# Optimization experiments

Measured on AMD Instinct MI355X. Metric: run time of the kernel, lower is better.

## Reference

```python
import jax, jax.numpy as jnp
import numpy as np

STEP = 16      # step_size
WIN = 8        # causal window width from attn_mask
NUM_HEADS = 4
LN_EPS = 1e-5


def conv1d(x, w, b, pad, dil):
    # x: [B, Cin, T], w: [Cout, Cin, K] (torch layout)
    y = jax.lax.conv_general_dilated(
        x, w, window_strides=(1,), padding=[(pad, pad)],
        rhs_dilation=(dil,), dimension_numbers=('NCH', 'OIH', 'NCH'))
    return y + b[None, :, None]


def temporal_block(x, w1, b1, w2, b2, wd, bd, dil, pad):
    # Canonical TCN block: conv->chomp->relu (dropout=eval noop) x2 + residual
    T = x.shape[-1]
    out = jax.nn.relu(conv1d(x, w1, b1, pad, dil)[..., :T])
    out = jax.nn.relu(conv1d(out, w2, b2, pad, dil)[..., :T])
    res = x if wd is None else conv1d(x, wd, bd, 0, 1)
    return jax.nn.relu(out + res)


def layer_norm(x, g, b):
    m = x.mean(-1, keepdims=True)
    v = x.var(-1, keepdims=True)
    return (x - m) / jnp.sqrt(v + LN_EPS) * g + b


def setup_inputs() -> dict:
    key = jax.random.key(0)
    NOISE, HID, B, T = 128, 256, 32, 4096
    ks = iter(jax.random.split(key, 48))
    rn = lambda shape, s=0.05: jax.random.normal(next(ks), shape, jnp.float32) * s
    inp = {'z': jax.random.normal(next(ks), (B, NOISE, T), jnp.float32)}
    # TCN block 0: kernel 1, noise_dim -> hidden_dim, with 1x1 downsample
    inp['tb0_w1'] = rn((HID, NOISE, 1)); inp['tb0_b1'] = jnp.zeros(HID)
    inp['tb0_w2'] = rn((HID, HID, 1));   inp['tb0_b2'] = jnp.zeros(HID)
    inp['tb0_wd'] = rn((HID, NOISE, 1)); inp['tb0_bd'] = jnp.zeros(HID)
    # TCN blocks 1..3: kernel 2, dilations 1,2,4, same channels (identity residual)
    for i in (1, 2, 3):
        inp[f'tb{i}_w1'] = rn((HID, HID, 2)); inp[f'tb{i}_b1'] = jnp.zeros(HID)
        inp[f'tb{i}_w2'] = rn((HID, HID, 2)); inp[f'tb{i}_b2'] = jnp.zeros(HID)
    # MultiheadAttention params (torch layout)
    inp['attn_in_w'] = rn((3 * HID, HID)); inp['attn_in_b'] = jnp.zeros(3 * HID)
    inp['attn_out_w'] = rn((HID, HID));    inp['attn_out_b'] = jnp.zeros(HID)
    inp['ln1_g'] = jnp.ones(HID); inp['ln1_b'] = jnp.zeros(HID)
    inp['ln2_g'] = jnp.ones(HID); inp['ln2_b'] = jnp.zeros(HID)
    inp['ffn_w1'] = rn((2 * HID, HID)); inp['ffn_b1'] = jnp.zeros(2 * HID)
    inp['ffn_w2'] = rn((HID, 2 * HID)); inp['ffn_b2'] = jnp.zeros(HID)
    inp['last_w'] = rn((1, HID)); inp['last_b'] = jnp.zeros(1)
    return inp


def reference(z, tb0_w1, tb0_b1, tb0_w2, tb0_b2, tb0_wd, tb0_bd,
              tb1_w1, tb1_b1, tb1_w2, tb1_b2,
              tb2_w1, tb2_b1, tb2_w2, tb2_b2,
              tb3_w1, tb3_b1, tb3_w2, tb3_b2,
              attn_in_w, attn_in_b, attn_out_w, attn_out_b,
              ln1_g, ln1_b, ln2_g, ln2_b,
              ffn_w1, ffn_b1, ffn_w2, ffn_b2,
              last_w, last_b):
    # --- TCN stack ---
    z = temporal_block(z, tb0_w1, tb0_b1, tb0_w2, tb0_b2, tb0_wd, tb0_bd, 1, 0)
    z = temporal_block(z, tb1_w1, tb1_b1, tb1_w2, tb1_b2, None, None, 1, 1)
    z = temporal_block(z, tb2_w1, tb2_b1, tb2_w2, tb2_b2, None, None, 2, 2)
    z = temporal_block(z, tb3_w1, tb3_b1, tb3_w2, tb3_b2, None, None, 4, 4)
    B, C, T = z.shape
    S = T // STEP
    # [B,C,S,STEP] -> [B,STEP,S,C] -> [B*STEP, S, C]
    x = z.reshape(B, C, S, STEP).transpose(0, 3, 2, 1).reshape(B * STEP, S, C)
    # --- causal sliding-window MHA ---
    qkv = x @ attn_in_w.T + attn_in_b
    q, k, v = jnp.split(qkv, 3, axis=-1)
    H, Dh = NUM_HEADS, C // NUM_HEADS
    heads = lambda t: t.reshape(B * STEP, S, H, Dh).transpose(0, 2, 1, 3)
    q, k, v = heads(q), heads(k), heads(v)
    scale = 1.0 / float(np.sqrt(Dh))
    scores = jnp.einsum('bhqd,bhkd->bhqk', q, k) * scale
    i = jnp.arange(S)[:, None]; j = jnp.arange(S)[None, :]
    allowed = (i - j >= 0) & (i - j < WIN)   # masked where i-j<0 or i-j>=8
    scores = jnp.where(allowed, scores, -jnp.inf)
    attn = jax.nn.softmax(scores, axis=-1)
    o = jnp.einsum('bhqk,bhkd->bhqd', attn, v)
    o = o.transpose(0, 2, 1, 3).reshape(B * STEP, S, C)
    o = o @ attn_out_w.T + attn_out_b
    # --- residual + LN + FFN + LN (dropout = eval noop) ---
    x = layer_norm(x + o, ln1_g, ln1_b)
    f = jax.nn.gelu(x @ ffn_w1.T + ffn_b1, approximate=False) @ ffn_w2.T + ffn_b2
    x = layer_norm(x + f, ln2_g, ln2_b)
    # un-fold back to [B, C, T]
    z = x.reshape(B, STEP, S, C).transpose(0, 3, 2, 1).reshape(B, C, T)
    out = z.transpose(0, 2, 1) @ last_w.T + last_b  # [B, T, 1]
    return out.transpose(0, 2, 1)                    # [B, 1, T]
```

## Files before the change

kernel.cpp:

```cpp
#include <hip/hip_runtime.h>
#include <cmath>

#define BB 32
#define TT 4096

typedef unsigned short u16;
typedef __attribute__((ext_vector_type(8))) __bf16 bf16x8;
typedef __attribute__((ext_vector_type(4))) float f32x4;
typedef __attribute__((ext_vector_type(8))) unsigned short u16x8;
typedef __attribute__((ext_vector_type(4))) unsigned short u16x4;
typedef __attribute__((ext_vector_type(2))) unsigned short u16x2;
typedef __attribute__((ext_vector_type(4))) unsigned int u32x4;

typedef __attribute__((address_space(3))) unsigned int lds_uint;
typedef __attribute__((address_space(1))) unsigned int g_uint;

__device__ __forceinline__ void gl_lds16(const void* g, void* l) {
    __builtin_amdgcn_global_load_lds((const g_uint*)g, (lds_uint*)l, 16, 0, 0);
}

__device__ __forceinline__ u16 f2b(float x) {
    unsigned u = __builtin_bit_cast(unsigned, x);
    return (u16)((u + 0x7fffu + ((u >> 16) & 1u)) >> 16);
}
__device__ __forceinline__ float b2f(u16 h) {
    unsigned u = ((unsigned)h) << 16;
    return __builtin_bit_cast(float, u);
}
__device__ __forceinline__ unsigned pkbf(float a, float b) {
    unsigned ua = __builtin_bit_cast(unsigned, a) + 0x8000u;
    unsigned ub = __builtin_bit_cast(unsigned, b) + 0x8000u;
    return __builtin_amdgcn_perm(ub, ua, 0x07060302);
}

enum : int {
  W_TB0_1 = 0,
  W_TB0_2 = 32768,
  W_TB0_D = 98304,
  W_TB1_1_T0 = 131072, W_TB1_1_T1 = 196608,
  W_TB1_2_T0 = 262144, W_TB1_2_T1 = 327680,
  W_TB2_1_T0 = 393216, W_TB2_1_T1 = 458752,
  W_TB2_2_T0 = 524288, W_TB2_2_T1 = 589824,
  W_TB3_1_T0 = 655360, W_TB3_1_T1 = 720896,
  W_TB3_2_T0 = 786432, W_TB3_2_T1 = 851968,
  W_ATTN_IN  = 917504,
  W_ATTN_OUT = 1114112,
  W_FFN1     = 1179648,
  W_FFN2     = 1310720,
};

__global__ __launch_bounds__(256)
void prep_weights(const float* s0, const float* s1, const float* s2,
                  const float* s3, const float* s4, const float* s5,
                  const float* s6, const float* s7, const float* s8,
                  const float* s9, const float* s10, const float* s11,
                  const float* s12, u16* wb)
{
    int seg = blockIdx.y;
    int i = blockIdx.x * 256 + threadIdx.x;
    switch (seg) {
    case 0:  if (i < 32768)  wb[W_TB0_1 + i] = f2b(s0[i]); break;
    case 1:  if (i < 65536)  wb[W_TB0_2 + i] = f2b(s1[i]); break;
    case 2:  if (i < 32768)  wb[W_TB0_D + i] = f2b(s2[i]); break;
    case 3:  if (i < 65536) { wb[W_TB1_1_T0 + i] = f2b(s3[2*i]); wb[W_TB1_1_T1 + i] = f2b(s3[2*i+1]); } break;
    case 4:  if (i < 65536) { wb[W_TB1_2_T0 + i] = f2b(s4[2*i]); wb[W_TB1_2_T1 + i] = f2b(s4[2*i+1]); } break;
    case 5:  if (i < 65536) { wb[W_TB2_1_T0 + i] = f2b(s5[2*i]); wb[W_TB2_1_T1 + i] = f2b(s5[2*i+1]); } break;
    case 6:  if (i < 65536) { wb[W_TB2_2_T0 + i] = f2b(s6[2*i]); wb[W_TB2_2_T1 + i] = f2b(s6[2*i+1]); } break;
    case 7:  if (i < 65536) { wb[W_TB3_1_T0 + i] = f2b(s7[2*i]); wb[W_TB3_1_T1 + i] = f2b(s7[2*i+1]); } break;
    case 8:  if (i < 65536) { wb[W_TB3_2_T0 + i] = f2b(s8[2*i]); wb[W_TB3_2_T1 + i] = f2b(s8[2*i+1]); } break;
    case 9:  if (i < 196608) wb[W_ATTN_IN + i]  = f2b(s9[i]);  break;
    case 10: if (i < 65536)  wb[W_ATTN_OUT + i] = f2b(s10[i]); break;
    case 11: if (i < 131072) wb[W_FFN1 + i]     = f2b(s11[i]); break;
    case 12: if (i < 131072) wb[W_FFN2 + i]     = f2b(s12[i]); break;
    }
}

__global__ __launch_bounds__(256)
void transpose_z(const float* __restrict__ z, u16* __restrict__ Z)
{
    __shared__ u16 tile[64][33];
    const int t0 = blockIdx.x << 6;
    const int c0 = blockIdx.y << 5;
    const int b  = blockIdx.z;
    const int tid = threadIdx.x;
    #pragma unroll
    for (int r = 0; r < 8; r++) {
        int lin = r * 256 + tid;
        int cc = lin >> 6, tt = lin & 63;
        tile[tt][cc] = f2b(z[((size_t)b * 128 + c0 + cc) * TT + t0 + tt]);
    }
    __syncthreads();
    #pragma unroll
    for (int r = 0; r < 8; r++) {
        int lin = r * 256 + tid;
        int tt = lin >> 5, cc = lin & 31;
        Z[((size_t)b * TT + t0 + tt) * 128 + c0 + cc] = tile[tt][cc];
    }
}

__device__ __forceinline__ const bf16x8* lds_frag(const u16* base, int row, int lc) {
    return (const bf16x8*)((const char*)base + row * 128 + (((lc ^ row) & 7) << 4) + ((lc & ~7) << 4));
}

template<int ACT, bool DUAL, int RMODE>
__global__ __launch_bounds__(256)
void gemm_tok(const u16* __restrict__ X, const u16* __restrict__ W1, int K,
              const u16* __restrict__ W2, int sh,
              const float* __restrict__ bias1,
              const u16* __restrict__ res, u16* __restrict__ Y, int M,
              const u16* __restrict__ zp)
{
    constexpr int XR = DUAL ? 132 : 128;
    constexpr int WR = DUAL ? 256 : 128;
    constexpr int WU = WR / 32;
    constexpr int STB = (XR + WR) * 128;
    constexpr int SMB = STB > 33792 ? STB : 33792;
    __shared__ __align__(16) char smem[SMB];
    u16* Xs = (u16*)smem;
    u16* Ws = (u16*)(smem + XR * 128);
    float (*CT)[132] = (float(*)[132])smem;

    const int tid = threadIdx.x;
    const int b  = blockIdx.z;
    const int t0 = blockIdx.x << 7;
    const int n0 = blockIdx.y << 7;
    const int lane = tid & 63;
    const int wv = tid >> 6;
    const int wt = (wv >> 1) << 6;
    const int wn = (wv & 1) << 6;
    const int l15 = lane & 15;
    const int quad = lane >> 4;
    const int shl = DUAL ? sh : 0;

    const char* xsrc[4]; char* xdst[4];
    #pragma unroll
    for (int u = 0; u < 4; u++) {
        const int c = tid + (u << 8);
        const int r = c >> 3, p = c & 7, q = p ^ (r & 7);
        const int st = t0 + r - shl;
        xdst[u] = (char*)Xs + c * 16;
        xsrc[u] = (const char*)((st >= 0 ? (X + ((size_t)b * TT + st) * K) : zp) + q * 8);
    }
    const char* wsrc[WU]; char* wdst[WU];
    #pragma unroll
    for (int u = 0; u < WU; u++) {
        const int c = tid + (u << 8);
        const int r = c >> 3, p = c & 7, q = p ^ (r & 7);
        wdst[u] = (char*)Ws + c * 16;
        const u16* wb_ = (DUAL && r >= 128) ? (W2 + (size_t)(n0 + r - 128) * K)
                                            : (W1 + (size_t)(n0 + r) * K);
        wsrc[u] = (const char*)(wb_ + q * 8);
    }
    const u16* hsrc = nullptr; u16* hdst = nullptr;
    if (DUAL && tid < 8 * shl) {
        const int hr = 128 + (tid >> 3), hp = tid & 7, hq = hp ^ (hr & 7);
        hsrc = X + ((size_t)b * TT + t0 + hr - shl) * K + hq * 8;
        hdst = (u16*)((char*)Xs + (1024 + tid) * 16);
    }

    f32x4 acc[4][4];
    #pragma unroll
    for (int j = 0; j < 4; j++) {
        const f32x4 bj = *(const f32x4*)&bias1[n0 + wn + j * 16 + quad * 4];
        #pragma unroll
        for (int i = 0; i < 4; i++) acc[i][j] = bj;
    }

    for (int k0 = 0; k0 < K; k0 += 64) {
        #pragma unroll
        for (int u = 0; u < 4; u++) gl_lds16(xsrc[u] + 2 * k0, xdst[u]);
        #pragma unroll
        for (int u = 0; u < WU; u++) gl_lds16(wsrc[u] + 2 * k0, wdst[u]);
        if (DUAL && hdst) *(u16x8*)hdst = *(const u16x8*)(hsrc + k0);
        __syncthreads();
        #pragma unroll
        for (int ks = 0; ks < 2; ks++) {
            bf16x8 af[4], bw[4];
            const int lc = ks * 4 + quad;
            #pragma unroll
            for (int i = 0; i < 4; i++)
                af[i] = *lds_frag(Xs, shl + wt + i * 16 + l15, lc);
            #pragma unroll
            for (int j = 0; j < 4; j++)
                bw[j] = *lds_frag(Ws, wn + j * 16 + l15, lc);
            #pragma unroll
            for (int i = 0; i < 4; i++)
                #pragma unroll
                for (int j = 0; j < 4; j++)
                    acc[i][j] = __builtin_amdgcn_mfma_f32_16x16x32_bf16(bw[j], af[i], acc[i][j], 0, 0, 0);
            if (DUAL) {
                #pragma unroll
                for (int i = 0; i < 4; i++)
                    af[i] = *lds_frag(Xs, wt + i * 16 + l15, lc);
                #pragma unroll
                for (int j = 0; j < 4; j++)
                    bw[j] = *lds_frag(Ws, 128 + wn + j * 16 + l15, lc);
                #pragma unroll
                for (int i = 0; i < 4; i++)
                    #pragma unroll
                    for (int j = 0; j < 4; j++)
                        acc[i][j] = __builtin_amdgcn_mfma_f32_16x16x32_bf16(bw[j], af[i], acc[i][j], 0, 0, 0);
            }
        }
        __syncthreads();
    }

    #pragma unroll
    for (int h = 0; h < 2; h++) {
        if (wt == h * 64) {
            #pragma unroll
            for (int i = 0; i < 4; i++) {
                const int tt = i * 16 + l15;
                #pragma unroll
                for (int j = 0; j < 4; j++)
                    *(f32x4*)&CT[tt][wn + j * 16 + quad * 4] = acc[i][j];
            }
        }
        __syncthreads();
        #pragma unroll
        for (int r4 = 0; r4 < 4; r4++) {
            const int lin = (r4 << 8) + tid;
            const int tt = lin >> 4;
            const int ck = lin & 15;
            const int gr = t0 + h * 64 + tt;
            const int gc = n0 + ck * 8;
            const size_t oidx = ((size_t)b * TT + gr) * M + gc;
            f32x4 v0 = *(const f32x4*)&CT[tt][ck * 8];
            f32x4 v1 = *(const f32x4*)&CT[tt][ck * 8 + 4];
            if (RMODE) {
                const u16x8 rv = *(const u16x8*)&res[oidx];
                if (RMODE == 2) {
                    #pragma unroll
                    for (int e = 0; e < 4; e++) {
                        v0[e] = fmaxf(fmaxf(v0[e], 0.f) + b2f(rv[e]), 0.f);
                        v1[e] = fmaxf(fmaxf(v1[e], 0.f) + b2f(rv[e + 4]), 0.f);
                    }
                } else {
                    #pragma unroll
                    for (int e = 0; e < 4; e++) { v0[e] += b2f(rv[e]); v1[e] += b2f(rv[e + 4]); }
                }
            }
            if (RMODE != 2) {
                if (ACT == 1) {
                    #pragma unroll
                    for (int e = 0; e < 4; e++) { v0[e] = fmaxf(v0[e], 0.f); v1[e] = fmaxf(v1[e], 0.f); }
                }
                if (ACT == 2) {
                    #pragma unroll
                    for (int e = 0; e < 4; e++) {
                        v0[e] = 0.5f * v0[e] * (1.f + erff(v0[e] * 0.70710678118f));
                        v1[e] = 0.5f * v1[e] * (1.f + erff(v1[e] * 0.70710678118f));
                    }
                }
            }
            u32x4 po;
            po[0] = pkbf(v0[0], v0[1]);
            po[1] = pkbf(v0[2], v0[3]);
            po[2] = pkbf(v1[0], v1[1]);
            po[3] = pkbf(v1[2], v1[3]);
            *(u32x4*)&Y[oidx] = po;
        }
        if (h == 0) __syncthreads();
    }
}

__global__ __launch_bounds__(256)
void attn_win(const u16* __restrict__ QKV, u16* __restrict__ O)
{
    __shared__ u16 KV[256 * 68];
    const int p = blockIdx.x, h = blockIdx.y, b = blockIdx.z;
    const int tid = threadIdx.x;
    const int s = tid;

    float qv[64];
    {
        size_t qg = ((size_t)b * TT + s * 16 + p) * 768 + h * 64;
        #pragma unroll
        for (int c = 0; c < 8; c++) {
            u16x8 u = *(const u16x8*)&QKV[qg + c * 8];
            #pragma unroll
            for (int j = 0; j < 8; j++) qv[c * 8 + j] = b2f(u[j]);
        }
    }
    for (int u = tid; u < 2048; u += 256) {
        int r = u >> 3, q = u & 7;
        size_t g = ((size_t)b * TT + r * 16 + p) * 768 + 256 + h * 64 + q * 8;
        u16x8 v = *(const u16x8*)&QKV[g];
        u16x4 lo = {v[0], v[1], v[2], v[3]}, hi = {v[4], v[5], v[6], v[7]};
        *(u16x4*)&KV[r * 68 + q * 8] = lo;
        *(u16x4*)&KV[r * 68 + q * 8 + 4] = hi;
    }
    __syncthreads();
    float sc[8];
    float mx = -1e30f;
    #pragma unroll
    for (int kk = 0; kk < 8; kk++) {
        int row = s - 7 + kk;
        float a = -1e30f;
        if (row >= 0) {
            a = 0.f;
            const u16* kr = &KV[row * 68];
            #pragma unroll
            for (int d = 0; d < 32; d++) {
                u16x2 u = *(const u16x2*)&kr[d * 2];
                a += qv[d * 2] * b2f(u[0]) + qv[d * 2 + 1] * b2f(u[1]);
            }
            a *= 0.125f;
        }
        sc[kk] = a;
        mx = fmaxf(mx, a);
    }
    float se = 0.f;
    #pragma unroll
    for (int kk = 0; kk < 8; kk++) {
        float e = (sc[kk] > -1e29f) ? __expf(sc[kk] - mx) : 0.f;
        sc[kk] = e; se += e;
    }
    const float inv = 1.f / se;
    __syncthreads();
    for (int u = tid; u < 2048; u += 256) {
        int r = u >> 3, q = u & 7;
        size_t g = ((size_t)b * TT + r * 16 + p) * 768 + 512 + h * 64 + q * 8;
        u16x8 v = *(const u16x8*)&QKV[g];
        u16x4 lo = {v[0], v[1], v[2], v[3]}, hi = {v[4], v[5], v[6], v[7]};
        *(u16x4*)&KV[r * 68 + q * 8] = lo;
        *(u16x4*)&KV[r * 68 + q * 8 + 4] = hi;
    }
    __syncthreads();
    float ov[64];
    #pragma unroll
    for (int d = 0; d < 64; d++) ov[d] = 0.f;
    #pragma unroll
    for (int kk = 0; kk < 8; kk++) {
        int row = s - 7 + kk;
        if (row >= 0) {
            float w = sc[kk] * inv;
            const u16* vr = &KV[row * 68];
            #pragma unroll
            for (int d = 0; d < 32; d++) {
                u16x2 u = *(const u16x2*)&vr[d * 2];
                ov[d * 2]     += w * b2f(u[0]);
                ov[d * 2 + 1] += w * b2f(u[1]);
            }
        }
    }
    size_t og = ((size_t)b * TT + s * 16 + p) * 256 + h * 64;
    #pragma unroll
    for (int d4 = 0; d4 < 16; d4++) {
        u16x4 o = {f2b(ov[d4 * 4]), f2b(ov[d4 * 4 + 1]), f2b(ov[d4 * 4 + 2]), f2b(ov[d4 * 4 + 3])};
        *(u16x4*)&O[og + d4 * 4] = o;
    }
}

__global__ __launch_bounds__(256)
void ln_fused(const u16* __restrict__ A, const u16* __restrict__ Bi,
              const float* __restrict__ g, const float* __restrict__ be,
              u16* __restrict__ Yo)
{
    const int row = blockIdx.x * 4 + (threadIdx.x >> 6);
    const int lane = threadIdx.x & 63;
    const size_t base = (size_t)row * 256 + lane * 4;
    u16x4 av = *(const u16x4*)&A[base];
    u16x4 bv = *(const u16x4*)&Bi[base];
    float v[4]; float sm = 0.f, sq = 0.f;
    #pragma unroll
    for (int j = 0; j < 4; j++) {
        v[j] = b2f(av[j]) + b2f(bv[j]);
        sm += v[j]; sq += v[j] * v[j];
    }
    #pragma unroll
    for (int off = 32; off >= 1; off >>= 1) {
        sm += __shfl_xor(sm, off, 64);
        sq += __shfl_xor(sq, off, 64);
    }
    const float mean = sm * (1.f / 256.f);
    const float var  = sq * (1.f / 256.f) - mean * mean;
    const float rstd = rsqrtf(var + 1e-5f);
    u16x4 o;
    #pragma unroll
    for (int j = 0; j < 4; j++) {
        float x = (v[j] - mean) * rstd * g[lane * 4 + j] + be[lane * 4 + j];
        o[j] = f2b(x);
    }
    *(u16x4*)&Yo[base] = o;
}

__global__ __launch_bounds__(256)
void ln_final(const u16* __restrict__ A, const u16* __restrict__ Bi,
              const float* __restrict__ g, const float* __restrict__ be,
              const float* __restrict__ lw, const float* __restrict__ lb,
              float* __restrict__ out)
{
    const int row = blockIdx.x * 4 + (threadIdx.x >> 6);
    const int lane = threadIdx.x & 63;
    const size_t base = (size_t)row * 256 + lane * 4;
    u16x4 av = *(const u16x4*)&A[base];
    u16x4 bv = *(const u16x4*)&Bi[base];
    float v[4]; float sm = 0.f, sq = 0.f;
    #pragma unroll
    for (int j = 0; j < 4; j++) {
        v[j] = b2f(av[j]) + b2f(bv[j]);
        sm += v[j]; sq += v[j] * v[j];
    }
    #pragma unroll
    for (int off = 32; off >= 1; off >>= 1) {
        sm += __shfl_xor(sm, off, 64);
        sq += __shfl_xor(sq, off, 64);
    }
    const float mean = sm * (1.f / 256.f);
    const float var  = sq * (1.f / 256.f) - mean * mean;
    const float rstd = rsqrtf(var + 1e-5f);
    const f32x4 gv = *(const f32x4*)&g[lane * 4];
    const f32x4 bev = *(const f32x4*)&be[lane * 4];
    const f32x4 lwv = *(const f32x4*)&lw[lane * 4];
    float a = 0.f;
    #pragma unroll
    for (int j = 0; j < 4; j++) {
        float x = (v[j] - mean) * rstd * gv[j] + bev[j];
        a += x * lwv[j];
    }
    #pragma unroll
    for (int off = 32; off >= 1; off >>= 1) a += __shfl_xor(a, off, 64);
    if (lane == 0) out[row] = a + lb[0];
}

extern "C" void kernel_launch(void* const* d_in, const int* in_sizes, int n_in,
                              void* d_out, int out_size, void* d_ws, size_t ws_size,
                              hipStream_t stream)
{
    const float* z        = (const float*)d_in[0];
    const float* tb0_b1   = (const float*)d_in[2];
    const float* tb0_b2   = (const float*)d_in[4];
    const float* tb0_bd   = (const float*)d_in[6];
    const float* tb1_b1   = (const float*)d_in[8];
    const float* tb1_b2   = (const float*)d_in[10];
    const float* tb2_b1   = (const float*)d_in[12];
    const float* tb2_b2   = (const float*)d_in[14];
    const float* tb3_b1   = (const float*)d_in[16];
    const float* tb3_b2   = (const float*)d_in[18];
    const float* attn_in_b  = (const float*)d_in[20];
    const float* attn_out_b = (const float*)d_in[22];
    const float* ln1_g = (const float*)d_in[23];
    const float* ln1_b = (const float*)d_in[24];
    const float* ln2_g = (const float*)d_in[25];
    const float* ln2_b = (const float*)d_in[26];
    const float* ffn_b1 = (const float*)d_in[28];
    const float* ffn_b2 = (const float*)d_in[30];
    const float* last_w = (const float*)d_in[31];
    const float* last_b = (const float*)d_in[32];
    (void)in_sizes; (void)n_in; (void)out_size;

    const size_t MB = 1ull << 20;
    int Bc = 0;
    for (int c = 32; c >= 1; c >>= 1) {
        if (ws_size >= (4 + 12 * (size_t)c) * MB) { Bc = c; break; }
    }
    if (Bc == 0) return;

    char* ws = (char*)d_ws;
    u16* WBp = (u16*)ws;
    u16* zp  = (u16*)(ws + 3 * MB);
    u16* U1  = (u16*)(ws + 4 * MB);
    u16* U2  = (u16*)(ws + (4 + 2 * (size_t)Bc) * MB);
    u16* U3  = (u16*)(ws + (4 + 4 * (size_t)Bc) * MB);
    u16* Q   = (u16*)(ws + (4 + 6 * (size_t)Bc) * MB);
    u16* Z   = Q;
    u16* F   = Q;
    float* outp = (float*)d_out;

    dim3 blk(256);
    hipMemsetAsync((void*)zp, 0, 4096, stream);
    prep_weights<<<dim3(768, 13), blk, 0, stream>>>(
        (const float*)d_in[1], (const float*)d_in[3], (const float*)d_in[5],
        (const float*)d_in[7], (const float*)d_in[9], (const float*)d_in[11],
        (const float*)d_in[13], (const float*)d_in[15], (const float*)d_in[17],
        (const float*)d_in[19], (const float*)d_in[21],
        (const float*)d_in[27], (const float*)d_in[29], WBp);

    const int nchunk = 32 / Bc;
    for (int c = 0; c < nchunk; c++) {
        const float* zc = z + (size_t)c * Bc * 128 * TT;
        float* oc = outp + (size_t)c * Bc * TT;

        transpose_z<<<dim3(64, 4, Bc), blk, 0, stream>>>(zc, Z);

        gemm_tok<1, false, 0><<<dim3(32, 2, Bc), blk, 0, stream>>>(Z, WBp + W_TB0_1, 128,
            nullptr, 0, tb0_b1, nullptr, U1, 256, zp);
        gemm_tok<1, false, 0><<<dim3(32, 2, Bc), blk, 0, stream>>>(U1, WBp + W_TB0_2, 256,
            nullptr, 0, tb0_b2, nullptr, U2, 256, zp);
        gemm_tok<1, false, 1><<<dim3(32, 2, Bc), blk, 0, stream>>>(Z, WBp + W_TB0_D, 128,
            nullptr, 0, tb0_bd, U2, U3, 256, zp);
        gemm_tok<1, true, 0><<<dim3(32, 2, Bc), blk, 0, stream>>>(U3, WBp + W_TB1_1_T1, 256,
            WBp + W_TB1_1_T0, 1, tb1_b1, nullptr, U1, 256, zp);
        gemm_tok<1, true, 2><<<dim3(32, 2, Bc), blk, 0, stream>>>(U1, WBp + W_TB1_2_T1, 256,
            WBp + W_TB1_2_T0, 1, tb1_b2, U3, U2, 256, zp);
        gemm_tok<1, true, 0><<<dim3(32, 2, Bc), blk, 0, stream>>>(U2, WBp + W_TB2_1_T1, 256,
            WBp + W_TB2_1_T0, 2, tb2_b1, nullptr, U1, 256, zp);
        gemm_tok<1, true, 2><<<dim3(32, 2, Bc), blk, 0, stream>>>(U1, WBp + W_TB2_2_T1, 256,
            WBp + W_TB2_2_T0, 2, tb2_b2, U2, U3, 256, zp);
        gemm_tok<1, true, 0><<<dim3(32, 2, Bc), blk, 0, stream>>>(U3, WBp + W_TB3_1_T1, 256,
            WBp + W_TB3_1_T0, 4, tb3_b1, nullptr, U1, 256, zp);
        gemm_tok<1, true, 2><<<dim3(32, 2, Bc), blk, 0, stream>>>(U1, WBp + W_TB3_2_T1, 256,
            WBp + W_TB3_2_T0, 4, tb3_b2, U3, U2, 256, zp);
        gemm_tok<0, false, 0><<<dim3(32, 6, Bc), blk, 0, stream>>>(U2, WBp + W_ATTN_IN, 256,
            nullptr, 0, attn_in_b, nullptr, Q, 768, zp);
        attn_win<<<dim3(16, 4, Bc), blk, 0, stream>>>(Q, U3);
        gemm_tok<0, false, 0><<<dim3(32, 2, Bc), blk, 0, stream>>>(U3, WBp + W_ATTN_OUT, 256,
            nullptr, 0, attn_out_b, nullptr, U1, 256, zp);
        ln_fused<<<dim3(Bc * 1024), blk, 0, stream>>>(U2, U1, ln1_g, ln1_b, U3);
        gemm_tok<2, false, 0><<<dim3(32, 4, Bc), blk, 0, stream>>>(U3, WBp + W_FFN1, 256,
            nullptr, 0, ffn_b1, nullptr, F, 512, zp);
        gemm_tok<0, false, 0><<<dim3(32, 2, Bc), blk, 0, stream>>>(F, WBp + W_FFN2, 512,
            nullptr, 0, ffn_b2, nullptr, U1, 256, zp);
        ln_final<<<dim3(Bc * 1024), blk, 0, stream>>>(U3, U1, ln2_g, ln2_b, last_w, last_b, oc);
    }
}
```

Measured before the change: 913.4 us.

## Fuse LayerNorm and final projection into full-row 128x256 GEMM epilogues

Adds a 512-thread GEMM kernel whose tile covers all 256 output channels of a token row. This lets the residual add, LayerNorm and final linear projection run in the GEMM epilogue, replacing the separate ln_fused and ln_final kernels and their extra activation round trips. The single-path GEMMs (TCN block 0, attention in/out, FFN) move to the wider tile, which also halves the number of blocks and re-reads of the X tile. The dual-tap conv GEMM is split into its own kernel. The larger tiles reduce grid size and may lower occupancy.

```diff
diff --git a/kernel.cpp b/kernel.cpp
--- a/kernel.cpp
+++ b/kernel.cpp
@@ -102,18 +102,181 @@
     return (const bf16x8*)((const char*)base + row * 128 + (((lc ^ row) & 7) << 4) + ((lc & ~7) << 4));
 }
 
-template<int ACT, bool DUAL, int RMODE>
+template<int ACT, int RMODE, int EPI>
+__global__ __launch_bounds__(512)
+void gemm512(const u16* __restrict__ X, const u16* __restrict__ W, int K, int M,
+             const float* __restrict__ bias,
+             const u16* __restrict__ res, u16* __restrict__ Y,
+             const float* __restrict__ g, const float* __restrict__ be,
+             const float* __restrict__ lw, const float* __restrict__ lb,
+             float* __restrict__ out)
+{
+    __shared__ __align__(16) char smem[49152];
+    u16* Xs = (u16*)smem;
+    u16* Ws = (u16*)(smem + 16384);
+    float (*CT)[260] = (float(*)[260])smem;
+
+    const int tid = threadIdx.x;
+    const int b  = blockIdx.z;
+    const int t0 = blockIdx.x << 7;
+    const int n0 = blockIdx.y << 8;
+    const int lane = tid & 63;
+    const int wv = tid >> 6;
+    const int wt = (wv >> 2) << 6;
+    const int wn = (wv & 3) << 6;
+    const int l15 = lane & 15;
+    const int quad = lane >> 4;
+
+    const char* xsrc[2]; char* xdst[2];
+    #pragma unroll
+    for (int u = 0; u < 2; u++) {
+        const int c = tid + (u << 9);
+        const int r = c >> 3, q = (c & 7) ^ (r & 7);
+        xdst[u] = (char*)Xs + c * 16;
+        xsrc[u] = (const char*)(X + ((size_t)b * TT + t0 + r) * K + q * 8);
+    }
+    const char* wsrc[4]; char* wdst[4];
+    #pragma unroll
+    for (int u = 0; u < 4; u++) {
+        const int c = tid + (u << 9);
+        const int r = c >> 3, q = (c & 7) ^ (r & 7);
+        wdst[u] = (char*)Ws + c * 16;
+        wsrc[u] = (const char*)(W + (size_t)(n0 + r) * K + q * 8);
+    }
+
+    f32x4 acc[4][4];
+    #pragma unroll
+    for (int j = 0; j < 4; j++) {
+        const f32x4 bj = *(const f32x4*)&bias[n0 + wn + j * 16 + quad * 4];
+        #pragma unroll
+        for (int i = 0; i < 4; i++) acc[i][j] = bj;
+    }
+
+    for (int k0 = 0; k0 < K; k0 += 64) {
+        #pragma unroll
+        for (int u = 0; u < 2; u++) gl_lds16(xsrc[u] + 2 * k0, xdst[u]);
+        #pragma unroll
+        for (int u = 0; u < 4; u++) gl_lds16(wsrc[u] + 2 * k0, wdst[u]);
+        __syncthreads();
+        #pragma unroll
+        for (int ks = 0; ks < 2; ks++) {
+            const int lc = ks * 4 + quad;
+            bf16x8 af[4], bw[4];
+            #pragma unroll
+            for (int i = 0; i < 4; i++)
+                af[i] = *lds_frag(Xs, wt + i * 16 + l15, lc);
+            #pragma unroll
+            for (int j = 0; j < 4; j++)
+                bw[j] = *lds_frag(Ws, wn + j * 16 + l15, lc);
+            #pragma unroll
+            for (int i = 0; i < 4; i++)
+                #pragma unroll
+                for (int j = 0; j < 4; j++)
+                    acc[i][j] = __builtin_amdgcn_mfma_f32_16x16x32_bf16(bw[j], af[i], acc[i][j], 0, 0, 0);
+        }
+        __syncthreads();
+    }
+
+    const int hsel = wv >> 2;
+    #pragma unroll
+    for (int h = 0; h < 4; h++) {
+        if ((h >> 1) == hsel) {
+            const int ibase = (h & 1) * 2;
+            #pragma unroll
+            for (int i2 = 0; i2 < 2; i2++) {
+                const int tt = i2 * 16 + l15;
+                #pragma unroll
+                for (int j = 0; j < 4; j++)
+                    *(f32x4*)&CT[tt][wn + j * 16 + quad * 4] = acc[ibase + i2][j];
+            }
+        }
+        __syncthreads();
+        #pragma unroll
+        for (int r2 = 0; r2 < 2; r2++) {
+            const int lin = (r2 << 9) + tid;
+            const int tt = lin >> 5;
+            const int ck = lin & 31;
+            const int token = t0 + h * 32 + tt;
+            const int gc = n0 + ck * 8;
+            f32x4 v0 = *(const f32x4*)&CT[tt][ck * 8];
+            f32x4 v1 = *(const f32x4*)&CT[tt][ck * 8 + 4];
+            if (RMODE == 1 || EPI >= 1) {
+                const u16x8 rv = *(const u16x8*)&res[((size_t)b * TT + token) * 256 + ck * 8];
+                #pragma unroll
+                for (int e = 0; e < 4; e++) { v0[e] += b2f(rv[e]); v1[e] += b2f(rv[e + 4]); }
+            }
+            if (EPI == 0) {
+                if (ACT == 1) {
+                    #pragma unroll
+                    for (int e = 0; e < 4; e++) { v0[e] = fmaxf(v0[e], 0.f); v1[e] = fmaxf(v1[e], 0.f); }
+                }
+                if (ACT == 2) {
+                    #pragma unroll
+                    for (int e = 0; e < 4; e++) {
+                        v0[e] = 0.5f * v0[e] * (1.f + erff(v0[e] * 0.70710678118f));
+                        v1[e] = 0.5f * v1[e] * (1.f + erff(v1[e] * 0.70710678118f));
+                    }
+                }
+                u32x4 po;
+                po[0] = pkbf(v0[0], v0[1]); po[1] = pkbf(v0[2], v0[3]);
+                po[2] = pkbf(v1[0], v1[1]); po[3] = pkbf(v1[2], v1[3]);
+                *(u32x4*)&Y[((size_t)b * TT + token) * M + gc] = po;
+            } else {
+                float s = 0.f, sq = 0.f;
+                #pragma unroll
+                for (int e = 0; e < 4; e++) {
+                    s += v0[e] + v1[e];
+                    sq += v0[e] * v0[e] + v1[e] * v1[e];
+                }
+                #pragma unroll
+                for (int off = 16; off >= 1; off >>= 1) {
+                    s += __shfl_xor(s, off, 64);
+                    sq += __shfl_xor(sq, off, 64);
+                }
+                const float mean = s * (1.f / 256.f);
+                const float var = sq * (1.f / 256.f) - mean * mean;
+                const float rstd = rsqrtf(var + 1e-5f);
+                const f32x4 g0 = *(const f32x4*)&g[gc];
+                const f32x4 g1 = *(const f32x4*)&g[gc + 4];
+                const f32x4 be0 = *(const f32x4*)&be[gc];
+                const f32x4 be1 = *(const f32x4*)&be[gc + 4];
+                f32x4 x0, x1;
+                #pragma unroll
+                for (int e = 0; e < 4; e++) {
+                    x0[e] = (v0[e] - mean) * rstd * g0[e] + be0[e];
+                    x1[e] = (v1[e] - mean) * rstd * g1[e] + be1[e];
+                }
+                if (EPI == 1) {
+                    u32x4 po;
+                    po[0] = pkbf(x0[0], x0[1]); po[1] = pkbf(x0[2], x0[3]);
+                    po[2] = pkbf(x1[0], x1[1]); po[3] = pkbf(x1[2], x1[3]);
+                    *(u32x4*)&Y[((size_t)b * TT + token) * 256 + gc] = po;
+                } else {
+                    const f32x4 w0 = *(const f32x4*)&lw[gc];
+                    const f32x4 w1 = *(const f32x4*)&lw[gc + 4];
+                    float a = 0.f;
+                    #pragma unroll
+                    for (int e = 0; e < 4; e++) a += x0[e] * w0[e] + x1[e] * w1[e];
+                    #pragma unroll
+                    for (int off = 16; off >= 1; off >>= 1) a += __shfl_xor(a, off, 64);
+                    if ((lane & 31) == 0) out[(size_t)b * TT + token] = a + lb[0];
+                }
+            }
+        }
+        __syncthreads();
+    }
+}
+
+template<int RMODE>
 __global__ __launch_bounds__(256)
-void gemm_tok(const u16* __restrict__ X, const u16* __restrict__ W1, int K,
-              const u16* __restrict__ W2, int sh,
-              const float* __restrict__ bias1,
-              const u16* __restrict__ res, u16* __restrict__ Y, int M,
-              const u16* __restrict__ zp)
+void gemm_dual(const u16* __restrict__ X, const u16* __restrict__ W1, int K,
+               const u16* __restrict__ W2, int sh,
+               const float* __restrict__ bias1,
+               const u16* __restrict__ res, u16* __restrict__ Y,
+               const u16* __restrict__ zp)
 {
-    constexpr int XR = DUAL ? 132 : 128;
-    constexpr int WR = DUAL ? 256 : 128;
-    constexpr int WU = WR / 32;
-    constexpr int STB = (XR + WR) * 128;
+    constexpr int XR = 132;
+    constexpr int STB = (XR + 256) * 128;
     constexpr int SMB = STB > 33792 ? STB : 33792;
     __shared__ __align__(16) char smem[SMB];
     u16* Xs = (u16*)smem;
@@ -130,7 +293,7 @@
     const int wn = (wv & 1) << 6;
     const int l15 = lane & 15;
     const int quad = lane >> 4;
-    const int shl = DUAL ? sh : 0;
+    const int shl = sh;
 
     const char* xsrc[4]; char* xdst[4];
     #pragma unroll
@@ -141,18 +304,18 @@
         xdst[u] = (char*)Xs + c * 16;
         xsrc[u] = (const char*)((st >= 0 ? (X + ((size_t)b * TT + st) * K) : zp) + q * 8);
     }
-    const char* wsrc[WU]; char* wdst[WU];
-    #pragma unroll
-    for (int u = 0; u < WU; u++) {
+    const char* wsrc[8]; char* wdst[8];
+    #pragma unroll
+    for (int u = 0; u < 8; u++) {
         const int c = tid + (u << 8);
         const int r = c >> 3, p = c & 7, q = p ^ (r & 7);
         wdst[u] = (char*)Ws + c * 16;
-        const u16* wb_ = (DUAL && r >= 128) ? (W2 + (size_t)(n0 + r - 128) * K)
-                                            : (W1 + (size_t)(n0 + r) * K);
+        const u16* wb_ = (r >= 128) ? (W2 + (size_t)(n0 + r - 128) * K)
+                                    : (W1 + (size_t)(n0 + r) * K);
         wsrc[u] = (const char*)(wb_ + q * 8);
     }
     const u16* hsrc = nullptr; u16* hdst = nullptr;
-    if (DUAL && tid < 8 * shl) {
+    if (tid < 8 * shl) {
         const int hr = 128 + (tid >> 3), hp = tid & 7, hq = hp ^ (hr & 7);
         hsrc = X + ((size_t)b * TT + t0 + hr - shl) * K + hq * 8;
         hdst = (u16*)((char*)Xs + (1024 + tid) * 16);
@@ -170,8 +333,8 @@
         #pragma unroll
         for (int u = 0; u < 4; u++) gl_lds16(xsrc[u] + 2 * k0, xdst[u]);
         #pragma unroll
-        for (int u = 0; u < WU; u++) gl_lds16(wsrc[u] + 2 * k0, wdst[u]);
-        if (DUAL && hdst) *(u16x8*)hdst = *(const u16x8*)(hsrc + k0);
+        for (int u = 0; u < 8; u++) gl_lds16(wsrc[u] + 2 * k0, wdst[u]);
+        if (hdst) *(u16x8*)hdst = *(const u16x8*)(hsrc + k0);
         __syncthreads();
         #pragma unroll
         for (int ks = 0; ks < 2; ks++) {
@@ -188,19 +351,17 @@
                 #pragma unroll
                 for (int j = 0; j < 4; j++)
                     acc[i][j] = __builtin_amdgcn_mfma_f32_16x16x32_bf16(bw[j], af[i], acc[i][j], 0, 0, 0);
-            if (DUAL) {
-                #pragma unroll
-                for (int i = 0; i < 4; i++)
-                    af[i] = *lds_frag(Xs, wt + i * 16 + l15, lc);
+            #pragma unroll
+            for (int i = 0; i < 4; i++)
+                af[i] = *lds_frag(Xs, wt + i * 16 + l15, lc);
+            #pragma unroll
+            for (int j = 0; j < 4; j++)
+                bw[j] = *lds_frag(Ws, 128 + wn + j * 16 + l15, lc);
+            #pragma unroll
+            for (int i = 0; i < 4; i++)
                 #pragma unroll
                 for (int j = 0; j < 4; j++)
-                    bw[j] = *lds_frag(Ws, 128 + wn + j * 16 + l15, lc);
-                #pragma unroll
-                for (int i = 0; i < 4; i++)
-                    #pragma unroll
-                    for (int j = 0; j < 4; j++)
-                        acc[i][j] = __builtin_amdgcn_mfma_f32_16x16x32_bf16(bw[j], af[i], acc[i][j], 0, 0, 0);
-            }
+                    acc[i][j] = __builtin_amdgcn_mfma_f32_16x16x32_bf16(bw[j], af[i], acc[i][j], 0, 0, 0);
         }
         __syncthreads();
     }
@@ -224,40 +385,23 @@
             const int ck = lin & 15;
             const int gr = t0 + h * 64 + tt;
             const int gc = n0 + ck * 8;
-            const size_t oidx = ((size_t)b * TT + gr) * M + gc;
+            const size_t oidx = ((size_t)b * TT + gr) * 256 + gc;
             f32x4 v0 = *(const f32x4*)&CT[tt][ck * 8];
             f32x4 v1 = *(const f32x4*)&CT[tt][ck * 8 + 4];
-            if (RMODE) {
+            if (RMODE == 2) {
                 const u16x8 rv = *(const u16x8*)&res[oidx];
-                if (RMODE == 2) {
-                    #pragma unroll
-                    for (int e = 0; e < 4; e++) {
-                        v0[e] = fmaxf(fmaxf(v0[e], 0.f) + b2f(rv[e]), 0.f);
-                        v1[e] = fmaxf(fmaxf(v1[e], 0.f) + b2f(rv[e + 4]), 0.f);
-                    }
-                } else {
-                    #pragma unroll
-                    for (int e = 0; e < 4; e++) { v0[e] += b2f(rv[e]); v1[e] += b2f(rv[e + 4]); }
-                }
-            }
-            if (RMODE != 2) {
-                if (ACT == 1) {
-                    #pragma unroll
-                    for (int e = 0; e < 4; e++) { v0[e] = fmaxf(v0[e], 0.f); v1[e] = fmaxf(v1[e], 0.f); }
-                }
-                if (ACT == 2) {
-                    #pragma unroll
-                    for (int e = 0; e < 4; e++) {
-                        v0[e] = 0.5f * v0[e] * (1.f + erff(v0[e] * 0.70710678118f));
-                        v1[e] = 0.5f * v1[e] * (1.f + erff(v1[e] * 0.70710678118f));
-                    }
-                }
+                #pragma unroll
+                for (int e = 0; e < 4; e++) {
+                    v0[e] = fmaxf(fmaxf(v0[e], 0.f) + b2f(rv[e]), 0.f);
+                    v1[e] = fmaxf(fmaxf(v1[e], 0.f) + b2f(rv[e + 4]), 0.f);
+                }
+            } else {
+                #pragma unroll
+                for (int e = 0; e < 4; e++) { v0[e] = fmaxf(v0[e], 0.f); v1[e] = fmaxf(v1[e], 0.f); }
             }
             u32x4 po;
-            po[0] = pkbf(v0[0], v0[1]);
-            po[1] = pkbf(v0[2], v0[3]);
-            po[2] = pkbf(v1[0], v1[1]);
-            po[3] = pkbf(v1[2], v1[3]);
+            po[0] = pkbf(v0[0], v0[1]); po[1] = pkbf(v0[2], v0[3]);
+            po[2] = pkbf(v1[0], v1[1]); po[3] = pkbf(v1[2], v1[3]);
             *(u32x4*)&Y[oidx] = po;
         }
         if (h == 0) __syncthreads();
@@ -350,78 +494,6 @@
         u16x4 o = {f2b(ov[d4 * 4]), f2b(ov[d4 * 4 + 1]), f2b(ov[d4 * 4 + 2]), f2b(ov[d4 * 4 + 3])};
         *(u16x4*)&O[og + d4 * 4] = o;
     }
-}
-
-__global__ __launch_bounds__(256)
-void ln_fused(const u16* __restrict__ A, const u16* __restrict__ Bi,
-              const float* __restrict__ g, const float* __restrict__ be,
-              u16* __restrict__ Yo)
-{
-    const int row = blockIdx.x * 4 + (threadIdx.x >> 6);
-    const int lane = threadIdx.x & 63;
-    const size_t base = (size_t)row * 256 + lane * 4;
-    u16x4 av = *(const u16x4*)&A[base];
-    u16x4 bv = *(const u16x4*)&Bi[base];
-    float v[4]; float sm = 0.f, sq = 0.f;
-    #pragma unroll
-    for (int j = 0; j < 4; j++) {
-        v[j] = b2f(av[j]) + b2f(bv[j]);
-        sm += v[j]; sq += v[j] * v[j];
-    }
-    #pragma unroll
-    for (int off = 32; off >= 1; off >>= 1) {
-        sm += __shfl_xor(sm, off, 64);
-        sq += __shfl_xor(sq, off, 64);
-    }
-    const float mean = sm * (1.f / 256.f);
-    const float var  = sq * (1.f / 256.f) - mean * mean;
-    const float rstd = rsqrtf(var + 1e-5f);
-    u16x4 o;
-    #pragma unroll
-    for (int j = 0; j < 4; j++) {
-        float x = (v[j] - mean) * rstd * g[lane * 4 + j] + be[lane * 4 + j];
-        o[j] = f2b(x);
-    }
-    *(u16x4*)&Yo[base] = o;
-}
-
-__global__ __launch_bounds__(256)
-void ln_final(const u16* __restrict__ A, const u16* __restrict__ Bi,
-              const float* __restrict__ g, const float* __restrict__ be,
-              const float* __restrict__ lw, const float* __restrict__ lb,
-              float* __restrict__ out)
-{
-    const int row = blockIdx.x * 4 + (threadIdx.x >> 6);
-    const int lane = threadIdx.x & 63;
-    const size_t base = (size_t)row * 256 + lane * 4;
-    u16x4 av = *(const u16x4*)&A[base];
-    u16x4 bv = *(const u16x4*)&Bi[base];
-    float v[4]; float sm = 0.f, sq = 0.f;
-    #pragma unroll
-    for (int j = 0; j < 4; j++) {
-        v[j] = b2f(av[j]) + b2f(bv[j]);
-        sm += v[j]; sq += v[j] * v[j];
-    }
-    #pragma unroll
-    for (int off = 32; off >= 1; off >>= 1) {
-        sm += __shfl_xor(sm, off, 64);
-        sq += __shfl_xor(sq, off, 64);
-    }
-    const float mean = sm * (1.f / 256.f);
-    const float var  = sq * (1.f / 256.f) - mean * mean;
-    const float rstd = rsqrtf(var + 1e-5f);
-    const f32x4 gv = *(const f32x4*)&g[lane * 4];
-    const f32x4 bev = *(const f32x4*)&be[lane * 4];
-    const f32x4 lwv = *(const f32x4*)&lw[lane * 4];
-    float a = 0.f;
-    #pragma unroll
-    for (int j = 0; j < 4; j++) {
-        float x = (v[j] - mean) * rstd * gv[j] + bev[j];
-        a += x * lwv[j];
-    }
-    #pragma unroll
-    for (int off = 32; off >= 1; off >>= 1) a += __shfl_xor(a, off, 64);
-    if (lane == 0) out[row] = a + lb[0];
 }
 
 extern "C" void kernel_launch(void* const* d_in, const int* in_sizes, int n_in,
@@ -468,9 +540,9 @@
     u16* F   = Q;
     float* outp = (float*)d_out;
 
-    dim3 blk(256);
+    dim3 b256(256), b512(512);
     hipMemsetAsync((void*)zp, 0, 4096, stream);
-    prep_weights<<<dim3(768, 13), blk, 0, stream>>>(
+    prep_weights<<<dim3(768, 13), b256, 0, stream>>>(
         (const float*)d_in[1], (const float*)d_in[3], (const float*)d_in[5],
         (const float*)d_in[7], (const float*)d_in[9], (const float*)d_in[11],
         (const float*)d_in[13], (const float*)d_in[15], (const float*)d_in[17],
@@ -482,36 +554,34 @@
         const float* zc = z + (size_t)c * Bc * 128 * TT;
         float* oc = outp + (size_t)c * Bc * TT;
 
-        transpose_z<<<dim3(64, 4, Bc), blk, 0, stream>>>(zc, Z);
-
-        gemm_tok<1, false, 0><<<dim3(32, 2, Bc), blk, 0, stream>>>(Z, WBp + W_TB0_1, 128,
-            nullptr, 0, tb0_b1, nullptr, U1, 256, zp);
-        gemm_tok<1, false, 0><<<dim3(32, 2, Bc), blk, 0, stream>>>(U1, WBp + W_TB0_2, 256,
-            nullptr, 0, tb0_b2, nullptr, U2, 256, zp);
-        gemm_tok<1, false, 1><<<dim3(32, 2, Bc), blk, 0, stream>>>(Z, WBp + W_TB0_D, 128,
-            nullptr, 0, tb0_bd, U2, U3, 256, zp);
-        gemm_tok<1, true, 0><<<dim3(32, 2, Bc), blk, 0, stream>>>(U3, WBp + W_TB1_1_T1, 256,
-            WBp + W_TB1_1_T0, 1, tb1_b1, nullptr, U1, 256, zp);
-        gemm_tok<1, true, 2><<<dim3(32, 2, Bc), blk, 0, stream>>>(U1, WBp + W_TB1_2_T1, 256,
-            WBp + W_TB1_2_T0, 1, tb1_b2, U3, U2, 256, zp);
-        gemm_tok<1, true, 0><<<dim3(32, 2, Bc), blk, 0, stream>>>(U2, WBp + W_TB2_1_T1, 256,
-            WBp + W_TB2_1_T0, 2, tb2_b1, nullptr, U1, 256, zp);
-        gemm_tok<1, true, 2><<<dim3(32, 2, Bc), blk, 0, stream>>>(U1, WBp + W_TB2_2_T1, 256,
-            WBp + W_TB2_2_T0, 2, tb2_b2, U2, U3, 256, zp);
-        gemm_tok<1, true, 0><<<dim3(32, 2, Bc), blk, 0, stream>>>(U3, WBp + W_TB3_1_T1, 256,
-            WBp + W_TB3_1_T0, 4, tb3_b1, nullptr, U1, 256, zp);
-        gemm_tok<1, true, 2><<<dim3(32, 2, Bc), blk, 0, stream>>>(U1, WBp + W_TB3_2_T1, 256,
-            WBp + W_TB3_2_T0, 4, tb3_b2, U3, U2, 256, zp);
-        gemm_tok<0, false, 0><<<dim3(32, 6, Bc), blk, 0, stream>>>(U2, WBp + W_ATTN_IN, 256,
-            nullptr, 0, attn_in_b, nullptr, Q, 768, zp);
-        attn_win<<<dim3(16, 4, Bc), blk, 0, stream>>>(Q, U3);
-        gemm_tok<0, false, 0><<<dim3(32, 2, Bc), blk, 0, stream>>>(U3, WBp + W_ATTN_OUT, 256,
-            nullptr, 0, attn_out_b, nullptr, U1, 256, zp);
-        ln_fused<<<dim3(Bc * 1024), blk, 0, stream>>>(U2, U1, ln1_g, ln1_b, U3);
-        gemm_tok<2, false, 0><<<dim3(32, 4, Bc), blk, 0, stream>>>(U3, WBp + W_FFN1, 256,
-            nullptr, 0, ffn_b1, nullptr, F, 512, zp);
-        gemm_tok<0, false, 0><<<dim3(32, 2, Bc), blk, 0, stream>>>(F, WBp + W_FFN2, 512,
-            nullptr, 0, ffn_b2, nullptr, U1, 256, zp);
-        ln_final<<<dim3(Bc * 1024), blk, 0, stream>>>(U3, U1, ln2_g, ln2_b, last_w, last_b, oc);
-    }
-}
+        transpose_z<<<dim3(64, 4, Bc), b256, 0, stream>>>(zc, Z);
+
+        gemm512<1, 0, 0><<<dim3(32, 1, Bc), b512, 0, stream>>>(Z, WBp + W_TB0_1, 128, 256,
+            tb0_b1, nullptr, U1, nullptr, nullptr, nullptr, nullptr, nullptr);
+        gemm512<1, 0, 0><<<dim3(32, 1, Bc), b512, 0, stream>>>(U1, WBp + W_TB0_2, 256, 256,
+            tb0_b2, nullptr, U2, nullptr, nullptr, nullptr, nullptr, nullptr);
+        gemm512<1, 1, 0><<<dim3(32, 1, Bc), b512, 0, stream>>>(Z, WBp + W_TB0_D, 128, 256,
+            tb0_bd, U2, U3, nullptr, nullptr, nullptr, nullptr, nullptr);
+        gemm_dual<0><<<dim3(32, 2, Bc), b256, 0, stream>>>(U3, WBp + W_TB1_1_T1, 256,
+            WBp + W_TB1_1_T0, 1, tb1_b1, nullptr, U1, zp);
+        gemm_dual<2><<<dim3(32, 2, Bc), b256, 0, stream>>>(U1, WBp + W_TB1_2_T1, 256,
+            WBp + W_TB1_2_T0, 1, tb1_b2, U3, U2, zp);
+        gemm_dual<0><<<dim3(32, 2, Bc), b256, 0, stream>>>(U2, WBp + W_TB2_1_T1, 256,
+            WBp + W_TB2_1_T0, 2, tb2_b1, nullptr, U1, zp);
+        gemm_dual<2><<<dim3(32, 2, Bc), b256, 0, stream>>>(U1, WBp + W_TB2_2_T1, 256,
+            WBp + W_TB2_2_T0, 2, tb2_b2, U2, U3, zp);
+        gemm_dual<0><<<dim3(32, 2, Bc), b256, 0, stream>>>(U3, WBp + W_TB3_1_T1, 256,
+            WBp + W_TB3_1_T0, 4, tb3_b1, nullptr, U1, zp);
+        gemm_dual<2><<<dim3(32, 2, Bc), b256, 0, stream>>>(U1, WBp + W_TB3_2_T1, 256,
+            WBp + W_TB3_2_T0, 4, tb3_b2, U3, U2, zp);
+        gemm512<0, 0, 0><<<dim3(32, 3, Bc), b512, 0, stream>>>(U2, WBp + W_ATTN_IN, 256, 768,
+            attn_in_b, nullptr, Q, nullptr, nullptr, nullptr, nullptr, nullptr);
+        attn_win<<<dim3(16, 4, Bc), b256, 0, stream>>>(Q, U3);
+        gemm512<0, 0, 1><<<dim3(32, 1, Bc), b512, 0, stream>>>(U3, WBp + W_ATTN_OUT, 256, 256,
+            attn_out_b, U2, U1, ln1_g, ln1_b, nullptr, nullptr, nullptr);
+        gemm512<2, 0, 0><<<dim3(32, 2, Bc), b512, 0, stream>>>(U1, WBp + W_FFN1, 256, 512,
+            ffn_b1, nullptr, F, nullptr, nullptr, nullptr, nullptr, nullptr);
+        gemm512<0, 0, 2><<<dim3(32, 1, Bc), b512, 0, stream>>>(F, WBp + W_FFN2, 512, 256,
+            ffn_b2, U1, nullptr, ln2_g, ln2_b, last_w, last_b, oc);
+    }
+}
```

Result: slower. 960.7 us (+5.2%).
